# Optimization experiments

Measured on AMD Instinct MI355X. Metric: run time of the kernel, lower is better.

Reference implementation:

```python
import jax, jax.numpy as jnp
import numpy as np
import math

DIM = 2048
N_HEADS = 16
HEAD_DIM = DIM // N_HEADS
BASE = 10000
B, S = 2, 2048


def rope_cache(seq_len, head_dim, base):
    theta = 1.0 / (base ** (jnp.arange(0, head_dim, 2, dtype=jnp.float32)[: head_dim // 2] / head_dim))
    idx_theta = jnp.arange(seq_len, dtype=jnp.float32)[:, None] * theta[None, :]  # [S, D/2]
    return jnp.cos(idx_theta), jnp.sin(idx_theta)


def apply_rope(x, cos, sin):
    # x: [B, S, H, D]; cos/sin: [S, D/2]; interleaved-pair rotation
    b, s, h, d = x.shape
    xr = x.astype(jnp.float32).reshape(b, s, h, d // 2, 2)
    c = cos[None, :, None, :]
    sn = sin[None, :, None, :]
    x0, x1 = xr[..., 0], xr[..., 1]
    out = jnp.stack([x0 * c - x1 * sn, x1 * c + x0 * sn], axis=-1)
    return out.reshape(b, s, h, d).astype(x.dtype)


def setup_inputs() -> dict:
    key = jax.random.key(0)
    k1, k2, k3, k4, k5 = jax.random.split(key, 5)
    x = jax.random.normal(k1, (B, S, DIM), dtype=jnp.float32)
    # causal mask: True = masked out (strict upper triangle)
    mask = jnp.triu(jnp.ones((S, S), dtype=bool), k=1)[None, None]  # [1,1,S,S]
    scale = 0.02
    wq = jax.random.normal(k2, (DIM, DIM), dtype=jnp.float32) * scale
    wk = jax.random.normal(k3, (DIM, DIM), dtype=jnp.float32) * scale
    wv = jax.random.normal(k4, (DIM, DIM), dtype=jnp.float32) * scale
    wo = jax.random.normal(k5, (DIM, DIM), dtype=jnp.float32) * scale
    return {"x": x, "mask": mask, "wq": wq, "wk": wk, "wv": wv, "wo": wo}


def reference(x, mask, wq, wk, wv, wo):
    b, s, _ = x.shape
    cos, sin = rope_cache(s, HEAD_DIM, BASE)
    q = (x @ wq.T).reshape(b, s, N_HEADS, HEAD_DIM)
    k = (x @ wk.T).reshape(b, s, N_HEADS, HEAD_DIM)
    v = (x @ wv.T).reshape(b, s, N_HEADS, HEAD_DIM)
    q = apply_rope(q, cos, sin)
    k = apply_rope(k, cos, sin)
    # [B, H, S, S]
    scores = jnp.einsum('bqhd,bkhd->bhqk', q, k) / math.sqrt(HEAD_DIM)
    scores = jnp.where(mask, -jnp.inf, scores)
    attn = jax.nn.softmax(scores.astype(jnp.float32), axis=-1).astype(q.dtype)
    out = jnp.einsum('bhqk,bkhd->bqhd', attn, v).reshape(b, s, DIM)
    return out @ wo.T
```

## Files before the change

kernel.cpp:

```cpp
#include <hip/hip_runtime.h>
#include <hip/hip_bf16.h>
#include <math.h>

#define DIM   2048
#define NH    16
#define HD    128
#define SEQ   2048
#define BATCH 2
#define QKVN  6144

typedef __attribute__((ext_vector_type(8))) short short8;
typedef __attribute__((ext_vector_type(4))) float f32x4;
typedef __attribute__((ext_vector_type(4))) unsigned int u32x4;
typedef __attribute__((ext_vector_type(4))) _Float16 half4;

static __device__ __forceinline__ unsigned short f2bf(float f) {
    __hip_bfloat16 h = __float2bfloat16(f);
    return *reinterpret_cast<unsigned short*>(&h);
}

static __device__ __forceinline__ void gload16(const void* g, void* l) {
    __builtin_amdgcn_global_load_lds(
        (const __attribute__((address_space(1))) void*)(g),
        (__attribute__((address_space(3))) void*)(l), 16, 0, 0);
}

__device__ __forceinline__ void storeC_helper(float* C, size_t idx, float v) { C[idx] = v; }
__device__ __forceinline__ void storeC_helper(__hip_bfloat16* C, size_t idx, float v) { C[idx] = __float2bfloat16(v); }

#define GFENCE()  asm volatile("" ::: "memory")
#define GBAR()    do { GFENCE(); __builtin_amdgcn_s_barrier(); GFENCE(); } while (0)
#define GWAITL0() do { asm volatile("s_waitcnt lgkmcnt(0)" ::: "memory"); __builtin_amdgcn_sched_barrier(0); } while (0)
#define GWAITV(n) asm volatile("s_waitcnt vmcnt(" n ")" ::: "memory")

__global__ __launch_bounds__(256) void cast_all(const float* __restrict__ x,
                                                const float* __restrict__ wq,
                                                const float* __restrict__ wk,
                                                const float* __restrict__ wv,
                                                const float* __restrict__ wo,
                                                __hip_bfloat16* __restrict__ xb,
                                                __hip_bfloat16* __restrict__ wqkvb,
                                                __hip_bfloat16* __restrict__ wob) {
    const int VX = (BATCH * SEQ * DIM) / 4;
    const int VW = (DIM * DIM) / 4;
    int v = blockIdx.x * blockDim.x + threadIdx.x;
    const float* src; __hip_bfloat16* dst; int off;
    if (v < VX)               { src = x;  dst = xb;                            off = v; }
    else if (v < VX + VW)     { src = wq; dst = wqkvb;                         off = v - VX; }
    else if (v < VX + 2 * VW) { src = wk; dst = wqkvb + (size_t)DIM * DIM;     off = v - VX - VW; }
    else if (v < VX + 3 * VW) { src = wv; dst = wqkvb + 2ull * DIM * DIM;      off = v - VX - 2 * VW; }
    else                      { src = wo; dst = wob;                           off = v - VX - 3 * VW; }
    float4 f = *(const float4*)(src + (size_t)off * 4);
    union { unsigned short u[4]; uint2 d; } pk;
    pk.u[0] = f2bf(f.x); pk.u[1] = f2bf(f.y); pk.u[2] = f2bf(f.z); pk.u[3] = f2bf(f.w);
    *(uint2*)(dst + (size_t)off * 4) = pk.d;
}

template <int MOFF>
static __device__ __forceinline__ void mfma16(const short8 (&af)[4], const short8 (&bf)[4],
                                              f32x4 (&acc)[8][4]) {
    __builtin_amdgcn_s_setprio(1);
#pragma unroll
    for (int mt = 0; mt < 4; mt++)
#pragma unroll
        for (int nt = 0; nt < 4; nt++)
            acc[MOFF + mt][nt] = __builtin_amdgcn_mfma_f32_16x16x32_bf16(
                af[mt], bf[nt], acc[MOFF + mt][nt], 0, 0, 0);
    __builtin_amdgcn_s_setprio(0);
}

__global__ __attribute__((amdgpu_waves_per_eu(2, 2))) __launch_bounds__(512)
void gemm256_qkv(const __hip_bfloat16* __restrict__ A,
                 const __hip_bfloat16* __restrict__ B,
                 __hip_bfloat16* __restrict__ C,
                 _Float16* __restrict__ vt) {
    constexpr int K  = DIM;
    constexpr int N  = QKVN;
    constexpr int NT = K / 64;
    constexpr int NI = NT / 2;
    __shared__ __align__(16) __hip_bfloat16 As[2][256 * 64];
    __shared__ __align__(16) __hip_bfloat16 Bs[2][256 * 64];

    int tid  = threadIdx.x;
    int lane = tid & 63;
    int wave = tid >> 6;
    int wm   = wave >> 2;
    int wn   = wave & 3;
    int quad = lane >> 4;
    int l15  = lane & 15;
    int m0   = blockIdx.y * 256;
    int n0   = blockIdx.x * 256;

    f32x4 acc[8][4] = {};

    auto stage = [&](int tau, int h) {
        const __hip_bfloat16* src;
        __hip_bfloat16* dst;
        if (h < 2) { src = A + (size_t)(m0 + h * 128) * K + tau * 64;
                     dst = &As[tau & 1][h * 8192]; }
        else       { src = B + (size_t)(n0 + (h - 2) * 128) * K + tau * 64;
                     dst = &Bs[tau & 1][(h - 2) * 8192]; }
#pragma unroll
        for (int c = 0; c < 2; c++) {
            int br = (wave * 2 + c) * 8;
            int r  = br + (lane >> 3);
            int cc = (lane & 7) ^ (r & 7);
            gload16(src + (size_t)r * K + cc * 8, dst + br * 64);
        }
    };

    int swz = l15 & 7;
    const __hip_bfloat16* a00 = &As[0][(wm * 128 + l15) * 64 + ((quad    ) ^ swz) * 8];
    const __hip_bfloat16* a01 = &As[0][(wm * 128 + l15) * 64 + ((4 + quad) ^ swz) * 8];
    const __hip_bfloat16* b00 = &Bs[0][(wn * 64  + l15) * 64 + ((quad    ) ^ swz) * 8];
    const __hip_bfloat16* b01 = &Bs[0][(wn * 64  + l15) * 64 + ((4 + quad) ^ swz) * 8];

    short8 aA[4], aB[4], aC[4], aD[4], bb0[4], bb1[4];

    stage(0, 0); stage(0, 1); stage(0, 2); stage(0, 3);
    stage(1, 0); stage(1, 1); stage(1, 2);
    GWAITV("6");
    GBAR();

#pragma unroll 1
    for (int i = 0; i < NI; i++) {
        const bool nl = (i < NI - 1);
#pragma unroll
        for (int t = 0; t < 4; t++) aA[t] = *(const short8*)(a00 + t * 1024);
#pragma unroll
        for (int t = 0; t < 4; t++) aB[t] = *(const short8*)(a00 + (4 + t) * 1024);
#pragma unroll
        for (int t = 0; t < 4; t++) bb0[t] = *(const short8*)(b00 + t * 1024);
        stage(2 * i + 1, 3);
        GBAR(); GWAITL0(); mfma16<0>(aA, bb0, acc); GBAR();
#pragma unroll
        for (int t = 0; t < 4; t++) aC[t] = *(const short8*)(a01 + t * 1024);
#pragma unroll
        for (int t = 0; t < 4; t++) aD[t] = *(const short8*)(a01 + (4 + t) * 1024);
#pragma unroll
        for (int t = 0; t < 4; t++) bb1[t] = *(const short8*)(b01 + t * 1024);
        GBAR(); GWAITL0(); mfma16<4>(aB, bb0, acc); GBAR();
        if (nl) stage(2 * i + 2, 0);
        GBAR(); GWAITL0(); mfma16<0>(aC, bb1, acc); GBAR();
        if (nl) stage(2 * i + 2, 1);
        GBAR(); GWAITL0(); mfma16<4>(aD, bb1, acc);
        if (nl) { GWAITV("4"); } else { GWAITV("0"); }
        GBAR();
#pragma unroll
        for (int t = 0; t < 4; t++) aA[t] = *(const short8*)(a00 + 16384 + t * 1024);
#pragma unroll
        for (int t = 0; t < 4; t++) aB[t] = *(const short8*)(a00 + 16384 + (4 + t) * 1024);
#pragma unroll
        for (int t = 0; t < 4; t++) bb0[t] = *(const short8*)(b00 + 16384 + t * 1024);
        if (nl) stage(2 * i + 2, 2);
        GBAR(); GWAITL0(); mfma16<0>(aA, bb0, acc); GBAR();
#pragma unroll
        for (int t = 0; t < 4; t++) aC[t] = *(const short8*)(a01 + 16384 + t * 1024);
#pragma unroll
        for (int t = 0; t < 4; t++) aD[t] = *(const short8*)(a01 + 16384 + (4 + t) * 1024);
#pragma unroll
        for (int t = 0; t < 4; t++) bb1[t] = *(const short8*)(b01 + 16384 + t * 1024);
        if (nl) stage(2 * i + 2, 3);
        GBAR(); GWAITL0(); mfma16<4>(aB, bb0, acc); GBAR();
        if (nl) { stage(2 * i + 3, 0); stage(2 * i + 3, 1); }
        GBAR(); GWAITL0(); mfma16<0>(aC, bb1, acc); GBAR();
        if (nl) stage(2 * i + 3, 2);
        GBAR(); GWAITL0(); mfma16<4>(aD, bb1, acc);
        if (nl) GWAITV("6");
        GBAR();
    }

    int ncol0 = n0 + wn * 64;
    if (ncol0 >= 4096) {
        _Float16* T = ((wave < 4) ? (_Float16*)As : (_Float16*)Bs) + (wave & 3) * 8192;
#pragma unroll
        for (int mt = 0; mt < 8; mt++)
#pragma unroll
            for (int nt = 0; nt < 4; nt++) {
                half4 hv;
#pragma unroll
                for (int r = 0; r < 4; r++) hv[r] = (_Float16)acc[mt][nt][r];
                int chunk = mt * 2 + (quad >> 1);
                int phys  = chunk ^ l15;
                *(half4*)(T + (nt * 16 + l15) * 128 + phys * 8 + (quad & 1) * 4) = hv;
            }
        int h  = (ncol0 - 4096) >> 7;
        int d0 = (ncol0 - 4096) & 127;
        int b  = (m0 + wm * 128) >> 11;
        int sb = (m0 + wm * 128) & (SEQ - 1);
#pragma unroll
        for (int pass = 0; pass < 16; pass++) {
            int d = pass * 4 + quad;
            int phys = l15 ^ (d & 15);
            u32x4 val = *(const u32x4*)(T + d * 128 + phys * 8);
            *(u32x4*)(vt + ((size_t)((b * NH + h) * HD + d0 + d)) * SEQ + sb + l15 * 8) = val;
        }
    } else {
#pragma unroll
        for (int nt = 0; nt < 4; nt++) {
            int col = ncol0 + nt * 16 + l15;
            float theta = __expf(-((float)((col & 127) & ~1) * (1.0f / (float)HD)) * 9.210340371976184f);
#pragma unroll
            for (int mt = 0; mt < 8; mt++)
#pragma unroll
                for (int r = 0; r < 4; r++) {
                    int row = m0 + wm * 128 + mt * 16 + quad * 4 + r;
                    float val = acc[mt][nt][r];
                    float part = __shfl_xor(val, 1);
                    int s = row & (SEQ - 1);
                    float sn, cs;
                    __sincosf((float)s * theta, &sn, &cs);
                    val = (l15 & 1) ? val * cs + part * sn : val * cs - part * sn;
                    C[(size_t)row * N + col] = __float2bfloat16(val);
                }
        }
    }
}

template <int MODE, typename OutT>
__global__ __launch_bounds__(256) void gemm_bt(const __hip_bfloat16* __restrict__ A,
                                               const __hip_bfloat16* __restrict__ B,
                                               OutT* __restrict__ C,
                                               _Float16* __restrict__ vt,
                                               int M, int N, int K) {
    constexpr int BK = 64;
    __shared__ __align__(16) __hip_bfloat16 As[128 * BK];
    __shared__ __align__(16) __hip_bfloat16 Bs[128 * BK];
    int tid  = threadIdx.x;
    int lane = tid & 63;
    int wave = tid >> 6;
    int quad = lane >> 4;
    int l15  = lane & 15;
    int wr   = wave >> 1, wc = wave & 1;
    int m0 = blockIdx.y * 128;
    int n0 = blockIdx.x * 128;
    f32x4 acc[4][4] = {};

    for (int k0 = 0; k0 < K; k0 += BK) {
        __syncthreads();
#pragma unroll
        for (int c = 0; c < 4; c++) {
            int br = (wave * 4 + c) * 8;
            int r  = br + (lane >> 3);
            int cc = (lane & 7) ^ (r & 7);
            gload16(A + (size_t)(m0 + r) * K + k0 + cc * 8, As + br * 64);
            gload16(B + (size_t)(n0 + r) * K + k0 + cc * 8, Bs + br * 64);
        }
        __syncthreads();
#pragma unroll
        for (int kk = 0; kk < BK; kk += 32) {
            short8 af[4], bf4[4];
#pragma unroll
            for (int t = 0; t < 4; t++) {
                int Ra = wr * 64 + t * 16 + l15;
                int pa = ((kk >> 3) + quad) ^ (Ra & 7);
                af[t] = *(const short8*)(As + Ra * 64 + pa * 8);
                int Rb = wc * 64 + t * 16 + l15;
                int pb = ((kk >> 3) + quad) ^ (Rb & 7);
                bf4[t] = *(const short8*)(Bs + Rb * 64 + pb * 8);
            }
#pragma unroll
            for (int mt = 0; mt < 4; mt++)
#pragma unroll
                for (int nt = 0; nt < 4; nt++)
                    acc[mt][nt] = __builtin_amdgcn_mfma_f32_16x16x32_bf16(af[mt], bf4[nt], acc[mt][nt], 0, 0, 0);
        }
    }

#pragma unroll
    for (int nt = 0; nt < 4; nt++) {
        int col = n0 + wc * 64 + nt * 16 + l15;
#pragma unroll
        for (int mt = 0; mt < 4; mt++)
#pragma unroll
            for (int r = 0; r < 4; r++) {
                int row = m0 + wr * 64 + mt * 16 + quad * 4 + r;
                storeC_helper(C, (size_t)row * N + col, acc[mt][nt][r]);
            }
    }
}

__global__ __launch_bounds__(512, 2) void flash_kernel(const __hip_bfloat16* __restrict__ qkv,
                                                       const _Float16* __restrict__ vt,
                                                       __hip_bfloat16* __restrict__ attn) {
    __shared__ __align__(16) __hip_bfloat16 Ks[2][2][64 * 128];
    __shared__ __align__(16) _Float16 Vts[2][2][128 * 64];
    int tid  = threadIdx.x;
    int lane = tid & 63;
    int wave = tid >> 6;
    int grp  = wave >> 2;
    int wl   = wave & 3;
    int quad = lane >> 4;
    int l15  = lane & 15;
    int pairi = blockIdx.x;
    int bh = blockIdx.y;
    int b  = bh >> 4;
    int h  = bh & 15;
    size_t row0 = (size_t)b * SEQ;
    const _Float16* vbase = vt + (size_t)bh * HD * SEQ;
    const float scale = 0.08838834764831845f;
    const float NEG = -1e30f;

    auto stage = [&](int buf, int kt) {
#pragma unroll
        for (int c = 0; c < 4; c++) {
            int br = (wl * 4 + c) * 4;
            int r  = br + (lane >> 4);
            int cc = (lane & 15) ^ (r & 15);
            gload16(qkv + (row0 + kt * 64 + r) * (size_t)QKVN + DIM + h * HD + cc * 8,
                    &Ks[grp][buf][br * 128]);
        }
#pragma unroll
        for (int c = 0; c < 4; c++) {
            int br = (wl * 4 + c) * 8;
            int r  = br + (lane >> 3);
            int cc = (lane & 7) ^ ((r >> 1) & 7);
            gload16(vbase + (size_t)r * SEQ + kt * 64 + cc * 8, &Vts[grp][buf][br * 64]);
        }
    };

    for (int seg = 0; seg < 2; seg++) {
        int qt = seg ? (15 - pairi) : pairi;
        int half = qt + 1;
        int kbase = grp ? half : 0;

        short8 qf[2][4];
#pragma unroll
        for (int mt = 0; mt < 2; mt++) {
            int qrow = qt * 128 + wl * 32 + mt * 16 + l15;
            const __hip_bfloat16* qptr = qkv + (row0 + qrow) * (size_t)QKVN + h * HD + quad * 8;
#pragma unroll
            for (int c = 0; c < 4; c++) qf[mt][c] = *(const short8*)(qptr + c * 32);
        }
        f32x4 o[2][8] = {};
        float m_[2] = {NEG, NEG}, l_[2] = {0.f, 0.f};

        stage(0, kbase);

        for (int i = 0; i < half; i++) {
            __syncthreads();
            if (i + 1 < half) stage((i + 1) & 1, kbase + i + 1);
            int kt = kbase + i;
            const __hip_bfloat16* ks = Ks[grp][i & 1];
            const _Float16* vts = Vts[grp][i & 1];

            f32x4 s[2][4] = {};
#pragma unroll
            for (int ktile = 0; ktile < 4; ktile++) {
                int R = ktile * 16 + l15;
#pragma unroll
                for (int c = 0; c < 4; c++) {
                    int phys = (c * 4 + quad) ^ (R & 15);
                    short8 kf = *(const short8*)(ks + R * 128 + phys * 8);
                    s[0][ktile] = __builtin_amdgcn_mfma_f32_16x16x32_bf16(kf, qf[0][c], s[0][ktile], 0, 0, 0);
                    s[1][ktile] = __builtin_amdgcn_mfma_f32_16x16x32_bf16(kf, qf[1][c], s[1][ktile], 0, 0, 0);
                }
            }
            bool diag = (kt >= 2 * qt);
            float alpha[2];
#pragma unroll
            for (int mt = 0; mt < 2; mt++) {
                int q = qt * 128 + wl * 32 + mt * 16 + l15;
#pragma unroll
                for (int ktile = 0; ktile < 4; ktile++)
#pragma unroll
                    for (int r = 0; r < 4; r++) {
                        float v = s[mt][ktile][r] * scale;
                        if (diag) {
                            int key = kt * 64 + ktile * 16 + quad * 4 + r;
                            if (key > q) v = NEG;
                        }
                        s[mt][ktile][r] = v;
                    }
                float v = s[mt][0][0];
#pragma unroll
                for (int ktile = 0; ktile < 4; ktile++)
#pragma unroll
                    for (int r = 0; r < 4; r++) v = fmaxf(v, s[mt][ktile][r]);
                v = fmaxf(v, __shfl_xor(v, 16));
                v = fmaxf(v, __shfl_xor(v, 32));
                float mnew = fmaxf(m_[mt], v);
                alpha[mt] = __expf(m_[mt] - mnew);
                m_[mt] = mnew;
                float sum = 0.f;
#pragma unroll
                for (int ktile = 0; ktile < 4; ktile++)
#pragma unroll
                    for (int r = 0; r < 4; r++) {
                        float p = __expf(s[mt][ktile][r] - mnew);
                        s[mt][ktile][r] = p;
                        sum += p;
                    }
                sum += __shfl_xor(sum, 16);
                sum += __shfl_xor(sum, 32);
                l_[mt] = l_[mt] * alpha[mt] + sum;
#pragma unroll
                for (int dt = 0; dt < 8; dt++) o[mt][dt] *= alpha[mt];
            }
            half4 pk[2][4];
#pragma unroll
            for (int mt = 0; mt < 2; mt++)
#pragma unroll
                for (int kc = 0; kc < 4; kc++)
#pragma unroll
                    for (int r = 0; r < 4; r++) pk[mt][kc][r] = (_Float16)s[mt][kc][r];
#pragma unroll
            for (int kc = 0; kc < 4; kc++)
#pragma unroll
                for (int dt = 0; dt < 8; dt++) {
                    int d = dt * 16 + l15;
                    int c4 = ((kc * 4 + quad) ^ (d & 14));
                    half4 vf = *(const half4*)(vts + d * 64 + c4 * 4);
                    o[0][dt] = __builtin_amdgcn_mfma_f32_16x16x16f16(vf, pk[0][kc], o[0][dt], 0, 0, 0);
                    o[1][dt] = __builtin_amdgcn_mfma_f32_16x16x16f16(vf, pk[1][kc], o[1][dt], 0, 0, 0);
                }
        }

        __syncthreads();
        float* o1mb = (float*)&Ks[0][0][0];
        float* mlmb = (float*)&Vts[0][0][0];
        __hip_bfloat16* tb = (__hip_bfloat16*)((char*)&Vts[0][0][0] + 8192);
        if (grp == 1) {
            float* dst = o1mb + wl * 4096;
#pragma unroll
            for (int mt = 0; mt < 2; mt++)
#pragma unroll
                for (int dt = 0; dt < 8; dt++)
#pragma unroll
                    for (int r = 0; r < 4; r++)
                        dst[((mt * 8 + dt) * 4 + r) * 64 + lane] = o[mt][dt][r];
            float* ml = mlmb + (wl * 64 + lane) * 4;
            ml[0] = m_[0]; ml[1] = m_[1]; ml[2] = l_[0]; ml[3] = l_[1];
        }
        __syncthreads();
        if (grp == 0) {
            const float* src = o1mb + wl * 4096;
            const float* ml = mlmb + (wl * 64 + lane) * 4;
#pragma unroll
            for (int mt = 0; mt < 2; mt++) {
                float m1 = ml[mt], l1 = ml[2 + mt];
                float mm = fmaxf(m_[mt], m1);
                float a0 = __expf(m_[mt] - mm), a1 = __expf(m1 - mm);
                float linv = 1.0f / (l_[mt] * a0 + l1 * a1);
#pragma unroll
                for (int dt = 0; dt < 8; dt++)
#pragma unroll
                    for (int r = 0; r < 4; r++)
                        o[mt][dt][r] = (o[mt][dt][r] * a0 +
                                        src[((mt * 8 + dt) * 4 + r) * 64 + lane] * a1) * linv;
            }
            __hip_bfloat16* tw = tb + wl * 4096;
#pragma unroll
            for (int mt = 0; mt < 2; mt++)
#pragma unroll
                for (int dt = 0; dt < 8; dt++) {
                    int q32 = mt * 16 + l15;
                    int c4 = dt * 4 + quad;
                    int phys = c4 ^ ((q32 & 7) << 2);
                    union { unsigned short u[4]; uint2 dw; } pkb;
#pragma unroll
                    for (int r = 0; r < 4; r++) pkb.u[r] = f2bf(o[mt][dt][r]);
                    *(uint2*)(tw + q32 * 128 + phys * 4) = pkb.dw;
                }
#pragma unroll
            for (int pass = 0; pass < 8; pass++) {
                int q32 = pass * 4 + (lane >> 4);
                int p = l15;
                int phys = (p * 2) ^ ((q32 & 7) << 2);
                u32x4 val = *(const u32x4*)(tw + q32 * 128 + phys * 4);
                int qg = qt * 128 + wl * 32 + q32;
                *(u32x4*)(attn + (row0 + qg) * (size_t)DIM + h * HD + p * 8) = val;
            }
        }
        __syncthreads();
    }
}

extern "C" void kernel_launch(void* const* d_in, const int* in_sizes, int n_in,
                              void* d_out, int out_size, void* d_ws, size_t ws_size,
                              hipStream_t stream) {
    const float* x  = (const float*)d_in[0];
    const float* wq = (const float*)d_in[2];
    const float* wk = (const float*)d_in[3];
    const float* wv = (const float*)d_in[4];
    const float* wo = (const float*)d_in[5];
    float* out = (float*)d_out;

    char* ws = (char*)d_ws;
    __hip_bfloat16* xb    = (__hip_bfloat16*)(ws);
    __hip_bfloat16* attn  = (__hip_bfloat16*)(ws);
    __hip_bfloat16* wqkvb = (__hip_bfloat16*)(ws + 16777216ull);
    __hip_bfloat16* wob   = (__hip_bfloat16*)(ws + 41943040ull);
    __hip_bfloat16* qkv   = (__hip_bfloat16*)(ws + 50331648ull);
    _Float16*       vtg   = (_Float16*)(ws + 100663296ull);

    const int nv = (BATCH * SEQ * DIM + 4 * DIM * DIM) / 4;
    cast_all<<<nv / 256, 256, 0, stream>>>(x, wq, wk, wv, wo, xb, wqkvb, wob);

    gemm256_qkv<<<dim3(QKVN / 256, (BATCH * SEQ) / 256), 512, 0, stream>>>(
        xb, wqkvb, qkv, vtg);

    flash_kernel<<<dim3(8, BATCH * NH), 512, 0, stream>>>(qkv, vtg, attn);

    gemm_bt<0, float><<<dim3(DIM / 128, (BATCH * SEQ) / 128), 256, 0, stream>>>(
        attn, wob, out, nullptr, BATCH * SEQ, DIM, DIM);
}
```

Baseline: 463.8 us.

## Reduce GEMM fragment registers and restage global-to-LDS prefetch schedule

Replaces the six sets of register fragments in the QKV projection GEMM main loop with two reused fragment buffers, loading A/B fragments just before each MFMA group. The prefetch schedule changes from keeping one and three-quarter stages of loads in flight to issuing the next half-tile's four chunks interleaved with compute and then waiting for all outstanding loads. The aim is to cut VGPR pressure, which could allow higher occupancy or avoid spills. In exchange, LDS reads are less batched ahead of the MFMAs and the full vmcnt(0) waits expose more global-load latency.

```diff
diff --git a/kernel.cpp b/kernel.cpp
--- a/kernel.cpp
+++ b/kernel.cpp
@@ -115,58 +115,56 @@
     const __hip_bfloat16* b00 = &Bs[0][(wn * 64  + l15) * 64 + ((quad    ) ^ swz) * 8];
     const __hip_bfloat16* b01 = &Bs[0][(wn * 64  + l15) * 64 + ((4 + quad) ^ swz) * 8];
 
-    short8 aA[4], aB[4], aC[4], aD[4], bb0[4], bb1[4];
+    short8 fa[4], fb[4];
 
     stage(0, 0); stage(0, 1); stage(0, 2); stage(0, 3);
-    stage(1, 0); stage(1, 1); stage(1, 2);
-    GWAITV("6");
+    GWAITV("0");
     GBAR();
 
 #pragma unroll 1
     for (int i = 0; i < NI; i++) {
         const bool nl = (i < NI - 1);
-#pragma unroll
-        for (int t = 0; t < 4; t++) aA[t] = *(const short8*)(a00 + t * 1024);
-#pragma unroll
-        for (int t = 0; t < 4; t++) aB[t] = *(const short8*)(a00 + (4 + t) * 1024);
-#pragma unroll
-        for (int t = 0; t < 4; t++) bb0[t] = *(const short8*)(b00 + t * 1024);
-        stage(2 * i + 1, 3);
-        GBAR(); GWAITL0(); mfma16<0>(aA, bb0, acc); GBAR();
-#pragma unroll
-        for (int t = 0; t < 4; t++) aC[t] = *(const short8*)(a01 + t * 1024);
-#pragma unroll
-        for (int t = 0; t < 4; t++) aD[t] = *(const short8*)(a01 + (4 + t) * 1024);
-#pragma unroll
-        for (int t = 0; t < 4; t++) bb1[t] = *(const short8*)(b01 + t * 1024);
-        GBAR(); GWAITL0(); mfma16<4>(aB, bb0, acc); GBAR();
+        stage(2 * i + 1, 2); stage(2 * i + 1, 3);
+#pragma unroll
+        for (int t = 0; t < 4; t++) fa[t] = *(const short8*)(a00 + t * 1024);
+#pragma unroll
+        for (int t = 0; t < 4; t++) fb[t] = *(const short8*)(b00 + t * 1024);
+        GBAR(); GWAITL0(); mfma16<0>(fa, fb, acc); GBAR();
+        stage(2 * i + 1, 0);
+#pragma unroll
+        for (int t = 0; t < 4; t++) fa[t] = *(const short8*)(a00 + (4 + t) * 1024);
+        GBAR(); GWAITL0(); mfma16<4>(fa, fb, acc); GBAR();
+        stage(2 * i + 1, 1);
+#pragma unroll
+        for (int t = 0; t < 4; t++) fa[t] = *(const short8*)(a01 + t * 1024);
+#pragma unroll
+        for (int t = 0; t < 4; t++) fb[t] = *(const short8*)(b01 + t * 1024);
+        GBAR(); GWAITL0(); mfma16<0>(fa, fb, acc); GBAR();
+#pragma unroll
+        for (int t = 0; t < 4; t++) fa[t] = *(const short8*)(a01 + (4 + t) * 1024);
+        GBAR(); GWAITL0(); mfma16<4>(fa, fb, acc);
+        GWAITV("0");
+        GBAR();
+        if (nl) { stage(2 * i + 2, 2); stage(2 * i + 2, 3); }
+#pragma unroll
+        for (int t = 0; t < 4; t++) fa[t] = *(const short8*)(a00 + 16384 + t * 1024);
+#pragma unroll
+        for (int t = 0; t < 4; t++) fb[t] = *(const short8*)(b00 + 16384 + t * 1024);
+        GBAR(); GWAITL0(); mfma16<0>(fa, fb, acc); GBAR();
         if (nl) stage(2 * i + 2, 0);
-        GBAR(); GWAITL0(); mfma16<0>(aC, bb1, acc); GBAR();
+#pragma unroll
+        for (int t = 0; t < 4; t++) fa[t] = *(const short8*)(a00 + 16384 + (4 + t) * 1024);
+        GBAR(); GWAITL0(); mfma16<4>(fa, fb, acc); GBAR();
         if (nl) stage(2 * i + 2, 1);
-        GBAR(); GWAITL0(); mfma16<4>(aD, bb1, acc);
-        if (nl) { GWAITV("4"); } else { GWAITV("0"); }
-        GBAR();
-#pragma unroll
-        for (int t = 0; t < 4; t++) aA[t] = *(const short8*)(a00 + 16384 + t * 1024);
-#pragma unroll
-        for (int t = 0; t < 4; t++) aB[t] = *(const short8*)(a00 + 16384 + (4 + t) * 1024);
-#pragma unroll
-        for (int t = 0; t < 4; t++) bb0[t] = *(const short8*)(b00 + 16384 + t * 1024);
-        if (nl) stage(2 * i + 2, 2);
-        GBAR(); GWAITL0(); mfma16<0>(aA, bb0, acc); GBAR();
-#pragma unroll
-        for (int t = 0; t < 4; t++) aC[t] = *(const short8*)(a01 + 16384 + t * 1024);
-#pragma unroll
-        for (int t = 0; t < 4; t++) aD[t] = *(const short8*)(a01 + 16384 + (4 + t) * 1024);
-#pragma unroll
-        for (int t = 0; t < 4; t++) bb1[t] = *(const short8*)(b01 + 16384 + t * 1024);
-        if (nl) stage(2 * i + 2, 3);
-        GBAR(); GWAITL0(); mfma16<4>(aB, bb0, acc); GBAR();
-        if (nl) { stage(2 * i + 3, 0); stage(2 * i + 3, 1); }
-        GBAR(); GWAITL0(); mfma16<0>(aC, bb1, acc); GBAR();
-        if (nl) stage(2 * i + 3, 2);
-        GBAR(); GWAITL0(); mfma16<4>(aD, bb1, acc);
-        if (nl) GWAITV("6");
+#pragma unroll
+        for (int t = 0; t < 4; t++) fa[t] = *(const short8*)(a01 + 16384 + t * 1024);
+#pragma unroll
+        for (int t = 0; t < 4; t++) fb[t] = *(const short8*)(b01 + 16384 + t * 1024);
+        GBAR(); GWAITL0(); mfma16<0>(fa, fb, acc); GBAR();
+#pragma unroll
+        for (int t = 0; t < 4; t++) fa[t] = *(const short8*)(a01 + 16384 + (4 + t) * 1024);
+        GBAR(); GWAITL0(); mfma16<4>(fa, fb, acc);
+        if (nl) GWAITV("0");
         GBAR();
     }
 
```

Result: faster. 414.4 us (-10.7%).
